# Performance work log

Measured on AMD Instinct MI355X. Metric: run time of the kernel, lower is better.

The kernel has to match this reference:

```python
import jax, jax.numpy as jnp
import numpy as np
from jax import lax

DN3D = ('NCDHW', 'OIDHW', 'NCDHW')


def conv4d_valid(x, w, b):
    """4D valid convolution, stride 1.
    x: [B, C, L, D, H, W]; w: [O, C, Lk, Dk, Hk, Wk]; b: [O].
    Implemented as a small fixed loop over the Lk kernel positions, each a
    batched 3D conv (L folded into batch) -- same math as torch Conv4d above.
    """
    B, C, L, D, H, W = x.shape
    O, _, Lk, Dk, Hk, Wk = w.shape
    Lo = L - Lk + 1
    out = None
    for i in range(Lk):
        xs = x[:, :, i:i + Lo]                      # [B, C, Lo, D, H, W]
        xs = xs.transpose(0, 2, 1, 3, 4, 5).reshape(B * Lo, C, D, H, W)
        o = lax.conv_general_dilated(xs, w[:, :, i], (1, 1, 1), 'VALID',
                                     dimension_numbers=DN3D)  # [B*Lo, O, Do, Ho, Wo]
        out = o if out is None else out + o
    _, _, Do, Ho, Wo = out.shape
    out = out.reshape(B, Lo, O, Do, Ho, Wo).transpose(0, 2, 1, 3, 4, 5)
    return out + b[None, :, None, None, None, None]


def setup_inputs() -> dict:
    key = jax.random.key(0)
    k0, k1, k2, k3, k4 = jax.random.split(key, 5)
    B = 16384
    return {
        'x': jax.random.normal(k0, (B, 1, 7, 7, 7, 7), dtype=jnp.float32),
        'w1': jax.random.normal(k1, (2, 1, 3, 3, 3, 3), dtype=jnp.float32) * 0.1,
        'b1': jax.random.normal(k2, (2,), dtype=jnp.float32) * 0.1,
        'w2': jax.random.normal(k3, (4, 2, 3, 3, 3, 3), dtype=jnp.float32) * 0.1,
        'b2': jax.random.normal(k4, (4,), dtype=jnp.float32) * 0.1,
    }


def reference(x, w1, b1, w2, b2):
    h = jax.nn.relu(conv4d_valid(x, w1, b1))   # [B, 2, 5, 5, 5, 5]
    h = jax.nn.relu(conv4d_valid(h, w2, b2))   # [B, 4, 3, 3, 3, 3]
    return h.reshape(h.shape[0], -1)           # [B, 324]
```

## Files before the change

### kernel.cpp

```cpp
#include <hip/hip_runtime.h>

#define SPB 4
#define TPB 256

__global__ __launch_bounds__(TPB, 2)
void conv4d_fused(const float* __restrict__ x,
                  const float* __restrict__ w1, const float* __restrict__ b1,
                  const float* __restrict__ w2, const float* __restrict__ b2,
                  float* __restrict__ out, int B)
{
    __shared__ float s_w1[162];
    __shared__ float s_w2[648];
    __shared__ float s_b1[2];
    __shared__ float s_b2[4];
    __shared__ float s_x[SPB * 2401];
    __shared__ float s_h1[SPB * 1250];

    const int t  = threadIdx.x;
    const int s0 = blockIdx.x * SPB;
    const int ns = min(SPB, B - s0);

    for (int i = t; i < 162; i += TPB) s_w1[i] = w1[i];
    for (int i = t; i < 648; i += TPB) s_w2[i] = w2[i];
    if (t < 2) s_b1[t] = b1[t];
    if (t < 4) s_b2[t] = b2[t];

    {
        const float* xp = x + (size_t)s0 * 2401;
        const int n = ns * 2401;
        for (int i = t; i < n; i += TPB) s_x[i] = xp[i];
    }
    __syncthreads();

    {
        const int ntask = ns * 50;
        if (t < ntask) {
            int s = t / 50;
            int r = t % 50;
            int o = r / 25; r %= 25;
            int l = r / 5, d = r % 5;

            float acc[5][5];
            const float bias = s_b1[o];
            #pragma unroll
            for (int h = 0; h < 5; ++h)
                #pragma unroll
                for (int w = 0; w < 5; ++w) acc[h][w] = bias;

            const float* xs = s_x + s * 2401;
            const float* wo = s_w1 + o * 81;
            #pragma unroll
            for (int kl = 0; kl < 3; ++kl)
            #pragma unroll
            for (int kd = 0; kd < 3; ++kd) {
                float p[7][7];
                const float* xp = xs + (l + kl) * 343 + (d + kd) * 49;
                #pragma unroll
                for (int i = 0; i < 49; ++i) p[i / 7][i % 7] = xp[i];
                const float* wp = wo + kl * 27 + kd * 9;
                #pragma unroll
                for (int kh = 0; kh < 3; ++kh)
                #pragma unroll
                for (int kw = 0; kw < 3; ++kw) {
                    const float wv = wp[kh * 3 + kw];
                    #pragma unroll
                    for (int h = 0; h < 5; ++h)
                    #pragma unroll
                    for (int w = 0; w < 5; ++w)
                        acc[h][w] += p[h + kh][w + kw] * wv;
                }
            }
            float* hp = s_h1 + s * 1250 + o * 625 + l * 125 + d * 25;
            #pragma unroll
            for (int h = 0; h < 5; ++h)
            #pragma unroll
            for (int w = 0; w < 5; ++w)
                hp[h * 5 + w] = fmaxf(acc[h][w], 0.0f);
        }
    }
    __syncthreads();

    {
        const int ntask = ns * 36;
        if (t < ntask) {
            int s = t / 36;
            int r = t % 36;
            int o2 = r / 9; r %= 9;
            int l = r / 3, d = r % 3;

            float acc[3][3];
            const float bias = s_b2[o2];
            #pragma unroll
            for (int h = 0; h < 3; ++h)
                #pragma unroll
                for (int w = 0; w < 3; ++w) acc[h][w] = bias;

            #pragma unroll
            for (int c = 0; c < 2; ++c) {
                const float* hs = s_h1 + s * 1250 + c * 625;
                const float* wb = s_w2 + o2 * 162 + c * 81;
                #pragma unroll
                for (int kl = 0; kl < 3; ++kl)
                #pragma unroll
                for (int kd = 0; kd < 3; ++kd) {
                    float p[5][5];
                    const float* pp = hs + (l + kl) * 125 + (d + kd) * 25;
                    #pragma unroll
                    for (int i = 0; i < 25; ++i) p[i / 5][i % 5] = pp[i];
                    const float* wp = wb + kl * 27 + kd * 9;
                    #pragma unroll
                    for (int kh = 0; kh < 3; ++kh)
                    #pragma unroll
                    for (int kw = 0; kw < 3; ++kw) {
                        const float wv = wp[kh * 3 + kw];
                        #pragma unroll
                        for (int h = 0; h < 3; ++h)
                        #pragma unroll
                        for (int w = 0; w < 3; ++w)
                            acc[h][w] += p[h + kh][w + kw] * wv;
                    }
                }
            }
            float* op = out + (size_t)(s0 + s) * 324 + o2 * 81 + l * 27 + d * 9;
            #pragma unroll
            for (int h = 0; h < 3; ++h)
            #pragma unroll
            for (int w = 0; w < 3; ++w)
                op[h * 3 + w] = fmaxf(acc[h][w], 0.0f);
        }
    }
}

extern "C" void kernel_launch(void* const* d_in, const int* in_sizes, int n_in,
                              void* d_out, int out_size, void* d_ws, size_t ws_size,
                              hipStream_t stream)
{
    const float* x  = (const float*)d_in[0];
    const float* w1 = (const float*)d_in[1];
    const float* b1 = (const float*)d_in[2];
    const float* w2 = (const float*)d_in[3];
    const float* b2 = (const float*)d_in[4];
    float* out = (float*)d_out;

    const int B = in_sizes[0] / 2401;
    const int grid = (B + SPB - 1) / SPB;
    conv4d_fused<<<grid, TPB, 0, stream>>>(x, w1, b1, w2, b2, out, B);
}
```

Measured before the change: 315.7 us.

## Pad shared layouts for float4 loads and alias h1 onto input buffer

Input planes in shared memory are padded to 52-float rows so each 7x7 plane can be read with 16-byte vector loads. The stage-1 output and the w2 weights now reuse the input buffer after a barrier instead of having their own arrays. The smaller shared footprint allows 5 samples per block and a launch bound of 3 blocks per SM, raising occupancy. The cost is an extra barrier, a scatter with a division during the input copy, and a tighter register budget.

```diff
diff --git a/kernel.cpp b/kernel.cpp
--- a/kernel.cpp
+++ b/kernel.cpp
@@ -1,133 +1,159 @@
 #include <hip/hip_runtime.h>
 
-#define SPB 4
+#define SPB 5
 #define TPB 256
+#define PS  52
+#define LS  364
+#define XS  2548
+#define H1P 28
+#define H1D 140
+#define H1O 700
+#define H1S 1400
+#define W2OFF 7000
 
-__global__ __launch_bounds__(TPB, 2)
+__global__ __launch_bounds__(TPB, 3)
 void conv4d_fused(const float* __restrict__ x,
                   const float* __restrict__ w1, const float* __restrict__ b1,
                   const float* __restrict__ w2, const float* __restrict__ b2,
                   float* __restrict__ out, int B)
 {
-    __shared__ float s_w1[162];
-    __shared__ float s_w2[648];
+    __shared__ __align__(16) float s_x[SPB * XS];
+    __shared__ __align__(16) float s_w1[164];
     __shared__ float s_b1[2];
     __shared__ float s_b2[4];
-    __shared__ float s_x[SPB * 2401];
-    __shared__ float s_h1[SPB * 1250];
 
     const int t  = threadIdx.x;
     const int s0 = blockIdx.x * SPB;
     const int ns = min(SPB, B - s0);
 
     for (int i = t; i < 162; i += TPB) s_w1[i] = w1[i];
-    for (int i = t; i < 648; i += TPB) s_w2[i] = w2[i];
     if (t < 2) s_b1[t] = b1[t];
     if (t < 4) s_b2[t] = b2[t];
 
     {
         const float* xp = x + (size_t)s0 * 2401;
-        const int n = ns * 2401;
-        for (int i = t; i < n; i += TPB) s_x[i] = xp[i];
+        for (int s = 0; s < ns; ++s) {
+            const float* xs = xp + s * 2401;
+            float* dst = s_x + s * XS;
+            for (int i = t; i < 2401; i += TPB) {
+                int p = (int)((unsigned)i / 49u);
+                dst[p * PS + (i - p * 49)] = xs[i];
+            }
+        }
     }
     __syncthreads();
 
-    {
-        const int ntask = ns * 50;
-        if (t < ntask) {
-            int s = t / 50;
-            int r = t % 50;
-            int o = r / 25; r %= 25;
-            int l = r / 5, d = r % 5;
+    float acc[5][5];
+    int p1_base = 0;
+    const bool act1 = t < ns * 50;
+    if (act1) {
+        int s = t / 50, r = t % 50;
+        int o = r / 25; r %= 25;
+        int l = r / 5, d = r % 5;
+        p1_base = s * H1S + o * H1O + l * H1D + d * H1P;
 
-            float acc[5][5];
-            const float bias = s_b1[o];
+        const float bias = s_b1[o];
+        #pragma unroll
+        for (int h = 0; h < 5; ++h)
             #pragma unroll
-            for (int h = 0; h < 5; ++h)
+            for (int w = 0; w < 5; ++w) acc[h][w] = bias;
+
+        const float* xs = s_x + s * XS;
+        const float* wo = s_w1 + o * 81;
+        #pragma unroll
+        for (int kl = 0; kl < 3; ++kl)
+        #pragma unroll
+        for (int kd = 0; kd < 3; ++kd) {
+            float pr[49];
+            const float4* q = (const float4*)(xs + (l + kl) * LS + (d + kd) * PS);
+            #pragma unroll
+            for (int v = 0; v < 12; ++v) {
+                float4 f = q[v];
+                pr[4 * v + 0] = f.x; pr[4 * v + 1] = f.y;
+                pr[4 * v + 2] = f.z; pr[4 * v + 3] = f.w;
+            }
+            pr[48] = ((const float*)q)[48];
+            const float* wp = wo + kl * 27 + kd * 9;
+            #pragma unroll
+            for (int kh = 0; kh < 3; ++kh)
+            #pragma unroll
+            for (int kw = 0; kw < 3; ++kw) {
+                const float wv = wp[kh * 3 + kw];
                 #pragma unroll
-                for (int w = 0; w < 5; ++w) acc[h][w] = bias;
+                for (int h = 0; h < 5; ++h)
+                #pragma unroll
+                for (int w = 0; w < 5; ++w)
+                    acc[h][w] += pr[(h + kh) * 7 + (w + kw)] * wv;
+            }
+        }
+    }
+    __syncthreads();
 
-            const float* xs = s_x + s * 2401;
-            const float* wo = s_w1 + o * 81;
+    if (act1) {
+        float4* hp4 = (float4*)(s_x + p1_base);
+        #pragma unroll
+        for (int v = 0; v < 6; ++v) {
+            float4 f;
+            f.x = fmaxf(acc[(4 * v + 0) / 5][(4 * v + 0) % 5], 0.0f);
+            f.y = fmaxf(acc[(4 * v + 1) / 5][(4 * v + 1) % 5], 0.0f);
+            f.z = fmaxf(acc[(4 * v + 2) / 5][(4 * v + 2) % 5], 0.0f);
+            f.w = fmaxf(acc[(4 * v + 3) / 5][(4 * v + 3) % 5], 0.0f);
+            hp4[v] = f;
+        }
+        s_x[p1_base + 24] = fmaxf(acc[4][4], 0.0f);
+    }
+    for (int i = t; i < 648; i += TPB) s_x[W2OFF + i] = w2[i];
+    __syncthreads();
+
+    if (t < ns * 36) {
+        int s = t / 36, r = t % 36;
+        int o2 = r / 9; r %= 9;
+        int l = r / 3, d = r % 3;
+
+        float a2[3][3];
+        const float bias = s_b2[o2];
+        #pragma unroll
+        for (int h = 0; h < 3; ++h)
+            #pragma unroll
+            for (int w = 0; w < 3; ++w) a2[h][w] = bias;
+
+        #pragma unroll
+        for (int c = 0; c < 2; ++c) {
+            const float* hs = s_x + s * H1S + c * H1O;
+            const float* wb = s_x + W2OFF + o2 * 162 + c * 81;
             #pragma unroll
             for (int kl = 0; kl < 3; ++kl)
             #pragma unroll
             for (int kd = 0; kd < 3; ++kd) {
-                float p[7][7];
-                const float* xp = xs + (l + kl) * 343 + (d + kd) * 49;
+                float pr[25];
+                const float4* q = (const float4*)(hs + (l + kl) * H1D + (d + kd) * H1P);
                 #pragma unroll
-                for (int i = 0; i < 49; ++i) p[i / 7][i % 7] = xp[i];
-                const float* wp = wo + kl * 27 + kd * 9;
+                for (int v = 0; v < 6; ++v) {
+                    float4 f = q[v];
+                    pr[4 * v + 0] = f.x; pr[4 * v + 1] = f.y;
+                    pr[4 * v + 2] = f.z; pr[4 * v + 3] = f.w;
+                }
+                pr[24] = ((const float*)q)[24];
+                const float* wp = wb + kl * 27 + kd * 9;
                 #pragma unroll
                 for (int kh = 0; kh < 3; ++kh)
                 #pragma unroll
                 for (int kw = 0; kw < 3; ++kw) {
                     const float wv = wp[kh * 3 + kw];
                     #pragma unroll
-                    for (int h = 0; h < 5; ++h)
+                    for (int h = 0; h < 3; ++h)
                     #pragma unroll
-                    for (int w = 0; w < 5; ++w)
-                        acc[h][w] += p[h + kh][w + kw] * wv;
+                    for (int w = 0; w < 3; ++w)
+                        a2[h][w] += pr[(h + kh) * 5 + (w + kw)] * wv;
                 }
             }
-            float* hp = s_h1 + s * 1250 + o * 625 + l * 125 + d * 25;
-            #pragma unroll
-            for (int h = 0; h < 5; ++h)
-            #pragma unroll
-            for (int w = 0; w < 5; ++w)
-                hp[h * 5 + w] = fmaxf(acc[h][w], 0.0f);
         }
-    }
-    __syncthreads();
-
-    {
-        const int ntask = ns * 36;
-        if (t < ntask) {
-            int s = t / 36;
-            int r = t % 36;
-            int o2 = r / 9; r %= 9;
-            int l = r / 3, d = r % 3;
-
-            float acc[3][3];
-            const float bias = s_b2[o2];
-            #pragma unroll
-            for (int h = 0; h < 3; ++h)
-                #pragma unroll
-                for (int w = 0; w < 3; ++w) acc[h][w] = bias;
-
-            #pragma unroll
-            for (int c = 0; c < 2; ++c) {
-                const float* hs = s_h1 + s * 1250 + c * 625;
-                const float* wb = s_w2 + o2 * 162 + c * 81;
-                #pragma unroll
-                for (int kl = 0; kl < 3; ++kl)
-                #pragma unroll
-                for (int kd = 0; kd < 3; ++kd) {
-                    float p[5][5];
-                    const float* pp = hs + (l + kl) * 125 + (d + kd) * 25;
-                    #pragma unroll
-                    for (int i = 0; i < 25; ++i) p[i / 5][i % 5] = pp[i];
-                    const float* wp = wb + kl * 27 + kd * 9;
-                    #pragma unroll
-                    for (int kh = 0; kh < 3; ++kh)
-                    #pragma unroll
-                    for (int kw = 0; kw < 3; ++kw) {
-                        const float wv = wp[kh * 3 + kw];
-                        #pragma unroll
-                        for (int h = 0; h < 3; ++h)
-                        #pragma unroll
-                        for (int w = 0; w < 3; ++w)
-                            acc[h][w] += p[h + kh][w + kw] * wv;
-                    }
-                }
-            }
-            float* op = out + (size_t)(s0 + s) * 324 + o2 * 81 + l * 27 + d * 9;
-            #pragma unroll
-            for (int h = 0; h < 3; ++h)
-            #pragma unroll
-            for (int w = 0; w < 3; ++w)
-                op[h * 3 + w] = fmaxf(acc[h][w], 0.0f);
-        }
+        float* op = out + (size_t)(s0 + s) * 324 + o2 * 81 + l * 27 + d * 9;
+        #pragma unroll
+        for (int h = 0; h < 3; ++h)
+        #pragma unroll
+        for (int w = 0; w < 3; ++w)
+            op[h * 3 + w] = fmaxf(a2[h][w], 0.0f);
     }
 }
 
```

Measured after the change: 371.8 us. 1.18x slower.
